# Optimization experiments

Measured on AMD Instinct MI355X. Metric: run time of the kernel, lower is better.

Reference implementation:

```python
import jax, jax.numpy as jnp
import numpy as np

N_NODES = 100000
N_EDGES = 1600000
IN_DIM = 128
HID = 128


def sage_conv(x, src, dst, W_l, W_r, b, num_nodes):
    # PyG SAGEConv (mean aggregation): out = lin_l(mean_{j in N(i)} x_j) + lin_r(x_i)
    msgs = x[src]                                            # [E, F] gather
    agg = jax.ops.segment_sum(msgs, dst, num_segments=num_nodes)  # [N, F]
    cnt = jax.ops.segment_sum(jnp.ones((src.shape[0],), x.dtype), dst,
                              num_segments=num_nodes)        # [N]
    agg = agg / jnp.maximum(cnt, 1.0)[:, None]               # mean; 0 for isolated nodes
    return agg @ W_l + b + x @ W_r


def setup_inputs() -> dict:
    key = jax.random.key(0)
    ks = jax.random.split(key, 12)
    s_in = 1.0 / np.sqrt(IN_DIM)
    s_h = 1.0 / np.sqrt(HID)
    return {
        "x": jax.random.normal(ks[0], (N_NODES, IN_DIM), jnp.float32),
        "edge_index": jax.random.randint(ks[1], (2, N_EDGES), 0, N_NODES, jnp.int64),
        "Wl1": jax.random.normal(ks[2], (IN_DIM, HID), jnp.float32) * s_in,
        "Wr1": jax.random.normal(ks[3], (IN_DIM, HID), jnp.float32) * s_in,
        "b1": jnp.zeros((HID,), jnp.float32),
        "Wl2": jax.random.normal(ks[4], (HID, HID), jnp.float32) * s_h,
        "Wr2": jax.random.normal(ks[5], (HID, HID), jnp.float32) * s_h,
        "b2": jnp.zeros((HID,), jnp.float32),
        "Wp": jax.random.normal(ks[6], (HID, 1), jnp.float32) * s_h,
        "bp": jnp.zeros((1,), jnp.float32),
        "Wd": jax.random.normal(ks[7], (HID, 1), jnp.float32) * s_h,
        "bd": jnp.zeros((1,), jnp.float32),
    }


def reference(x, edge_index, Wl1, Wr1, b1, Wl2, Wr2, b2, Wp, bp, Wd, bd):
    src, dst = edge_index[0], edge_index[1]
    h = jax.nn.relu(sage_conv(x, src, dst, Wl1, Wr1, b1, N_NODES))
    h = jax.nn.relu(sage_conv(h, src, dst, Wl2, Wr2, b2, N_NODES))
    preds = h @ Wp + bp                      # [N, 1]
    diffs = jax.nn.sigmoid(h @ Wd + bd)      # [N, 1]
    return (preds - diffs, preds + diffs)
```

## Files before the change

kernel.cpp:

```cpp
#include <hip/hip_runtime.h>
#include <hip/hip_bf16.h>

#define N_NODES 100000
#define N_EDGES 1600000
#define NBUCK 391
#define BCAP 5120
#define ACHUNK 4096

typedef __bf16 bf16x8 __attribute__((ext_vector_type(8)));
typedef __bf16 bf16x4 __attribute__((ext_vector_type(4)));
typedef float  f32x4  __attribute__((ext_vector_type(4)));
typedef float  f32x2  __attribute__((ext_vector_type(2)));



__global__ __launch_bounds__(512) void zerob_kernel(int* __restrict__ bcnt,
                                                    int* __restrict__ Psent) {
  int t = threadIdx.x;
  if (t < NBUCK) bcnt[t] = 0;
  if (t >= 480) Psent[t - 480] = 0;
}

__global__ __launch_bounds__(256) void partA_kernel(const int* __restrict__ src,
                                                    const int* __restrict__ dst,
                                                    int* __restrict__ bcnt,
                                                    unsigned* __restrict__ packed, int E) {
  __shared__ int hist[NBUCK];
  __shared__ int curs[NBUCK];
  const int t = threadIdx.x;
  for (int i = t; i < NBUCK; i += 256) hist[i] = 0;
  __syncthreads();

  const int base = blockIdx.x * ACHUNK;
  const int lim = min(base + ACHUNK, E);

  int dloc[16], sloc[16];
  int myn = 0;
  for (int i = base + t; i < lim; i += 256) {
    dloc[myn] = dst[i];
    sloc[myn] = src[i];
    ++myn;
  }
  for (int k = 0; k < myn; ++k) atomicAdd(&hist[dloc[k] >> 8], 1);
  __syncthreads();

  for (int i = t; i < NBUCK; i += 256) {
    int h = hist[i];
    curs[i] = (h > 0) ? atomicAdd(&bcnt[i], h) : 0;
  }
  __syncthreads();

  for (int k = 0; k < myn; ++k) {
    int d = dloc[k];
    int b = d >> 8;
    int pos = atomicAdd(&curs[b], 1);
    if (pos < BCAP)
      packed[(size_t)b * BCAP + pos] = ((unsigned)sloc[k] << 8) | (unsigned)(d & 255);
  }
}

__global__ __launch_bounds__(256) void partBh_kernel(const unsigned* __restrict__ packed,
                                                     const int* __restrict__ bcnt,
                                                     int* __restrict__ pcnt,
                                                     int* __restrict__ deg,
                                                     int* __restrict__ pbt, int N) {
  __shared__ int hist[256];
  __shared__ int red[256];
  const int b = blockIdx.x, t = threadIdx.x;
  hist[t] = 0;
  __syncthreads();
  const int ecnt = min(bcnt[b], BCAP);
  const unsigned* pk = packed + (size_t)b * BCAP;
  for (int i = t; i < ecnt; i += 256) atomicAdd(&hist[pk[i] & 255u], 1);
  __syncthreads();
  int c = hist[t];
  int node = b * 256 + t;
  int pc = (node < N) ? ((c + 3) & ~3) : 0;
  if (node < N) { deg[node] = c; pcnt[node] = pc; }
  red[t] = pc;
  __syncthreads();
  for (int d = 128; d > 0; d >>= 1) {
    if (t < d) red[t] += red[t + d];
    __syncthreads();
  }
  if (t == 0) pbt[b] = red[0];
}

__global__ __launch_bounds__(512) void bscan_kernel(const int* __restrict__ pbt,
                                                    int* __restrict__ bbase,
                                                    int* __restrict__ offs, int N) {
  __shared__ int tmp[512];
  int t = threadIdx.x;
  int v = (t < NBUCK) ? pbt[t] : 0;
  int x = v;
  tmp[t] = x;
  __syncthreads();
  for (int d = 1; d < 512; d <<= 1) {
    int y = (t >= d) ? tmp[t - d] : 0;
    __syncthreads();
    x += y;
    tmp[t] = x;
    __syncthreads();
  }
  if (t < NBUCK) bbase[t] = x - v;
  if (t == NBUCK - 1) offs[N] = x;
}

__global__ __launch_bounds__(256) void partBs_kernel(const unsigned* __restrict__ packed,
                                                     const int* __restrict__ bcnt,
                                                     const int* __restrict__ bbase,
                                                     const int* __restrict__ pcnt,
                                                     const int* __restrict__ deg,
                                                     int* __restrict__ offs,
                                                     int* __restrict__ ssrc, int N) {
  __shared__ int scanbuf[256];
  __shared__ int curs[256];
  const int b = blockIdx.x, t = threadIdx.x;
  const int node = b * 256 + t;
  int pc = (node < N) ? pcnt[node] : 0;
  int c  = (node < N) ? deg[node] : 0;
  int x = pc;
  scanbuf[t] = x;
  __syncthreads();
  for (int d = 1; d < 256; d <<= 1) {
    int y = (t >= d) ? scanbuf[t - d] : 0;
    __syncthreads();
    x += y;
    scanbuf[t] = x;
    __syncthreads();
  }
  int excl = x - pc;
  const int obase = bbase[b];
  if (node < N) offs[node] = obase + excl;
  curs[t] = excl;
  __syncthreads();

  const int ecnt = min(bcnt[b], BCAP);
  const unsigned* pk = packed + (size_t)b * BCAP;
  for (int i = t; i < ecnt; i += 256) {
    unsigned p = pk[i];
    int r = atomicAdd(&curs[p & 255u], 1);
    ssrc[obase + r] = (int)(p >> 8);
  }
  for (int j = c; j < pc; ++j) ssrc[obase + excl + j] = N;
}


__global__ __launch_bounds__(256) void wswz_kernel(const float* __restrict__ Wl1,
                                                   const float* __restrict__ Wr1,
                                                   const float* __restrict__ Wl2,
                                                   const float* __restrict__ Wr2,
                                                   __bf16* __restrict__ W1out,
                                                   __bf16* __restrict__ W2out) {
  int gi = blockIdx.x * blockDim.x + threadIdx.x;
  bool L2 = gi >= 32768;
  int i = gi & 32767;
  int j = i & 7;
  int lane = (i >> 3) & 63;
  int c = (i >> 9) & 3;
  int tile = i >> 11;
  int k = c * 32 + ((lane >> 4) * 8) + j;
  int krow = L2 ? (((k & 7) << 4) | (k >> 3)) : k;
  int col = tile * 16 + (lane & 15);
  const float* Wl = L2 ? Wl2 : Wl1;
  const float* Wr = L2 ? Wr2 : Wr1;
  float v = (col < 128) ? Wl[krow * 128 + col] : Wr[krow * 128 + (col - 128)];
  (L2 ? W2out : W1out)[i] = (__bf16)v;
}


template <bool A_IS_F32>
__global__ __launch_bounds__(256, 2) void gemm_kernel(const void* __restrict__ Aptr,
                                                      const __bf16* __restrict__ Wswz,
                                                      const float* __restrict__ bias,
                                                      unsigned char* __restrict__ P,
                                                      __bf16* __restrict__ R, int M,
                                                      int tiles, int stride) {
  const int t = threadIdx.x;
  const int lane = t & 63;
  const int w = t >> 6;
  const int q = lane >> 4;
  const int s = lane & 15;

  bf16x8 bfrag[16];
#pragma unroll
  for (int ct = 0; ct < 4; ++ct)
#pragma unroll
    for (int c = 0; c < 4; ++c)
      bfrag[ct * 4 + c] =
          *(const bf16x8*)&Wswz[(size_t)((((w * 4 + ct) * 4 + c) * 64) + lane) * 8];

  float breg[4];
#pragma unroll
  for (int j = 0; j < 4; ++j)
    breg[j] = (w >= 2) ? bias[((w - 2) * 4 + j) * 16 + s] : 0.f;

  for (int tile = blockIdx.x; tile < tiles; tile += stride) {
    const int m0 = tile * 64;

    bf16x8 afrag[16];
    if (A_IS_F32) {
      const float* A = (const float*)Aptr;
#pragma unroll
      for (int rt = 0; rt < 4; ++rt) {
        int rc = min(m0 + rt * 16 + s, M - 1);
#pragma unroll
        for (int c = 0; c < 4; ++c) {
          const float* p = &A[(size_t)rc * 128 + c * 32 + q * 8];
          float4 v0 = *(const float4*)p;
          float4 v1 = *(const float4*)(p + 4);
          bf16x8 a;
          a[0] = (__bf16)v0.x; a[1] = (__bf16)v0.y; a[2] = (__bf16)v0.z; a[3] = (__bf16)v0.w;
          a[4] = (__bf16)v1.x; a[5] = (__bf16)v1.y; a[6] = (__bf16)v1.z; a[7] = (__bf16)v1.w;
          afrag[rt * 4 + c] = a;
        }
      }
    } else {
      const __bf16* A = (const __bf16*)Aptr;
#pragma unroll
      for (int rt = 0; rt < 4; ++rt) {
        int rc = min(m0 + rt * 16 + s, M - 1);
#pragma unroll
        for (int c = 0; c < 4; ++c)
          afrag[rt * 4 + c] = *(const bf16x8*)&A[(size_t)rc * 128 + c * 32 + q * 8];
      }
    }

    f32x4 acc[16];
    f32x4 zero = {0.f, 0.f, 0.f, 0.f};
#pragma unroll
    for (int i = 0; i < 16; ++i) acc[i] = zero;

#pragma unroll
    for (int c = 0; c < 4; ++c)
#pragma unroll
      for (int rt = 0; rt < 4; ++rt)
#pragma unroll
        for (int ct = 0; ct < 4; ++ct)
          acc[rt * 4 + ct] = __builtin_amdgcn_mfma_f32_16x16x32_bf16(
              afrag[rt * 4 + c], bfrag[ct * 4 + c], acc[rt * 4 + ct], 0, 0, 0);

#pragma unroll
    for (int rt = 0; rt < 4; ++rt) {
#pragma unroll
      for (int r = 0; r < 4; ++r) {
        int row = m0 + rt * 16 + q * 4 + r;
        if (row < M) {
          if (w < 2) {
            unsigned v = 0;
            v = __builtin_amdgcn_cvt_pk_fp8_f32(acc[rt * 4 + 0][r], acc[rt * 4 + 1][r], v, false);
            v = __builtin_amdgcn_cvt_pk_fp8_f32(acc[rt * 4 + 2][r], acc[rt * 4 + 3][r], v, true);
            *(unsigned*)&P[(size_t)row * 128 + s * 8 + w * 4] = v;
          } else {
            bf16x4 o;
#pragma unroll
            for (int ct = 0; ct < 4; ++ct) o[ct] = (__bf16)(acc[rt * 4 + ct][r] + breg[ct]);
            *(bf16x4*)&R[(size_t)row * 128 + s * 8 + (w - 2) * 4] = o;
          }
        }
      }
    }
  }
}


template <bool FINAL>
__global__ __launch_bounds__(256) void agg_kernel(
    const unsigned char* __restrict__ P, const __bf16* R,
    const int* __restrict__ offs, const int* __restrict__ deg,
    const int* __restrict__ ssrc,
    __bf16* H, float* __restrict__ out,
    const float* __restrict__ Wp, const float* __restrict__ Wd,
    const float* __restrict__ bp, const float* __restrict__ bd, int n) {
  int w4 = (int)((blockIdx.x * blockDim.x + threadIdx.x) >> 6);
  int lane = threadIdx.x & 63;
  int g = lane >> 4;
  int s = lane & 15;
  int node = w4 * 4 + g;
  int nc = min(node, n - 1);
  int start = offs[nc];
  int pend = offs[nc + 1];

  f32x2 a01 = {0.f, 0.f}, a23 = {0.f, 0.f}, a45 = {0.f, 0.f}, a67 = {0.f, 0.f};

  const unsigned char* Pb = P + (size_t)s * 8;
  for (int cur = start; cur < pend; cur += 4) {
    uint4 sv = *(const uint4*)&ssrc[cur];
    uint2 v0 = *(const uint2*)(Pb + (size_t)sv.x * 128);
    uint2 v1 = *(const uint2*)(Pb + (size_t)sv.y * 128);
    uint2 v2 = *(const uint2*)(Pb + (size_t)sv.z * 128);
    uint2 v3 = *(const uint2*)(Pb + (size_t)sv.w * 128);
    a01 += __builtin_amdgcn_cvt_pk_f32_fp8(v0.x, false);
    a23 += __builtin_amdgcn_cvt_pk_f32_fp8(v0.x, true);
    a45 += __builtin_amdgcn_cvt_pk_f32_fp8(v0.y, false);
    a67 += __builtin_amdgcn_cvt_pk_f32_fp8(v0.y, true);
    a01 += __builtin_amdgcn_cvt_pk_f32_fp8(v1.x, false);
    a23 += __builtin_amdgcn_cvt_pk_f32_fp8(v1.x, true);
    a45 += __builtin_amdgcn_cvt_pk_f32_fp8(v1.y, false);
    a67 += __builtin_amdgcn_cvt_pk_f32_fp8(v1.y, true);
    a01 += __builtin_amdgcn_cvt_pk_f32_fp8(v2.x, false);
    a23 += __builtin_amdgcn_cvt_pk_f32_fp8(v2.x, true);
    a45 += __builtin_amdgcn_cvt_pk_f32_fp8(v2.y, false);
    a67 += __builtin_amdgcn_cvt_pk_f32_fp8(v2.y, true);
    a01 += __builtin_amdgcn_cvt_pk_f32_fp8(v3.x, false);
    a23 += __builtin_amdgcn_cvt_pk_f32_fp8(v3.x, true);
    a45 += __builtin_amdgcn_cvt_pk_f32_fp8(v3.y, false);
    a67 += __builtin_amdgcn_cvt_pk_f32_fp8(v3.y, true);
  }

  int dg = deg[nc];
  float inv = 1.0f / (float)(dg > 0 ? dg : 1);

  bf16x8 rv = *(const bf16x8*)&R[(size_t)nc * 128 + s * 8];
  float acc[8] = {a01[0], a01[1], a23[0], a23[1], a45[0], a45[1], a67[0], a67[1]};
  float h[8];
#pragma unroll
  for (int j = 0; j < 8; ++j) {
    h[j] = fmaxf(acc[j] * inv + (float)rv[j], 0.f);
  }

  if (!FINAL) {
    if (node < n) {
      bf16x8 o;
#pragma unroll
      for (int j = 0; j < 8; ++j) o[j] = (__bf16)h[j];
      *(bf16x8*)&H[(size_t)node * 128 + s * 8] = o;
    }
  } else {
    float p = 0.f, dd = 0.f;
#pragma unroll
    for (int j = 0; j < 8; ++j) {
      p += h[j] * Wp[j * 16 + s];
      dd += h[j] * Wd[j * 16 + s];
    }
    p += __shfl_xor(p, 1, 64);  p += __shfl_xor(p, 2, 64);
    p += __shfl_xor(p, 4, 64);  p += __shfl_xor(p, 8, 64);
    dd += __shfl_xor(dd, 1, 64); dd += __shfl_xor(dd, 2, 64);
    dd += __shfl_xor(dd, 4, 64); dd += __shfl_xor(dd, 8, 64);
    if (node < n && s == 0) {
      float preds = p + bp[0];
      float sg = 1.0f / (1.0f + __expf(-(dd + bd[0])));
      out[node] = preds - sg;
      out[n + node] = preds + sg;
    }
  }
}


extern "C" void kernel_launch(void* const* d_in, const int* in_sizes, int n_in,
                              void* d_out, int out_size, void* d_ws, size_t ws_size,
                              hipStream_t stream) {
  const float* x    = (const float*)d_in[0];
  const int*   ei   = (const int*)d_in[1];
  const float* Wl1 = (const float*)d_in[2];
  const float* Wr1 = (const float*)d_in[3];
  const float* b1  = (const float*)d_in[4];
  const float* Wl2 = (const float*)d_in[5];
  const float* Wr2 = (const float*)d_in[6];
  const float* b2  = (const float*)d_in[7];
  const float* Wp  = (const float*)d_in[8];
  const float* bp  = (const float*)d_in[9];
  const float* Wd  = (const float*)d_in[10];
  const float* bd  = (const float*)d_in[11];
  float* out = (float*)d_out;

  const int N = N_NODES, E = N_EDGES;
  const int* src = ei;
  const int* dst = ei + E;
  const size_t PADE = (size_t)E + 3 * (size_t)N + 64;

  char* w = (char*)d_ws;
  unsigned char* P = (unsigned char*)w; w += (size_t)(N + 1) * 128;
  __bf16* R1     = (__bf16*)w;   w += (size_t)N * 128 * 2;
  __bf16* R2     = (__bf16*)w;   w += (size_t)N * 128 * 2;
  int* ssrc      = (int*)w;      w += PADE * 4;
  unsigned* pck  = (unsigned*)w; w += (size_t)NBUCK * BCAP * 4;
  int* bcnt      = (int*)w;      w += 512 * 4;
  int* bbase     = (int*)w;      w += 512 * 4;
  int* pbt       = (int*)w;      w += 512 * 4;
  int* pcnt      = (int*)w;      w += (size_t)(N + 32) * 4;
  int* deg       = (int*)w;      w += (size_t)(N + 32) * 4;
  int* offs      = (int*)w;      w += (size_t)(N + 32) * 4;
  __bf16* Ws1    = (__bf16*)w;   w += 65536;
  __bf16* Ws2    = (__bf16*)w;   w += 65536;

  zerob_kernel<<<1, 512, 0, stream>>>(bcnt, (int*)(P + (size_t)N * 128));
  wswz_kernel<<<256, 256, 0, stream>>>(Wl1, Wr1, Wl2, Wr2, Ws1, Ws2);
  partA_kernel<<<(E + ACHUNK - 1) / ACHUNK, 256, 0, stream>>>(src, dst, bcnt, pck, E);
  partBh_kernel<<<NBUCK, 256, 0, stream>>>(pck, bcnt, pcnt, deg, pbt, N);
  bscan_kernel<<<1, 512, 0, stream>>>(pbt, bbase, offs, N);
  partBs_kernel<<<NBUCK, 256, 0, stream>>>(pck, bcnt, bbase, pcnt, deg, offs, ssrc, N);

  const int TILES = (N + 63) / 64;
  const int GG = 512;
  const int AB = (N + 15) / 16;
  gemm_kernel<true><<<GG, 256, 0, stream>>>(x, Ws1, b1, P, R1, N, TILES, GG);
  agg_kernel<false><<<AB, 256, 0, stream>>>(P, R1, offs, deg, ssrc, R1, nullptr,
                                            nullptr, nullptr, nullptr, nullptr, N);
  gemm_kernel<false><<<GG, 256, 0, stream>>>(R1, Ws2, b2, P, R2, N, TILES, GG);
  agg_kernel<true><<<AB, 256, 0, stream>>>(P, R2, offs, deg, ssrc, nullptr, out,
                                           Wp, Wd, bp, bd, N);
}
```

Baseline: 278.9 us.

## Fuse layer-1 aggregation with layer-2 GEMM and stage GEMM1 inputs through LDS

Layer-1 neighbour aggregation and the layer-2 linear transform now run in one persistent kernel. Each block aggregates 16 nodes, stages the hidden rows in LDS and feeds them to MFMA, so the bf16 hidden matrix is never written to or read back from global memory, and one launch disappears. The gather loop issues two groups of 4 neighbour loads per iteration to keep more loads in flight. The first GEMM now loads its fp32 input tile cooperatively into LDS with coalesced float4 reads before building fragments. The trade-off is that the fused kernel runs at launch bound 2 with a fixed 512-block grid-stride, which may leave fewer waves to hide the latency of the random gathers.

```diff
diff --git a/kernel.cpp b/kernel.cpp
--- a/kernel.cpp
+++ b/kernel.cpp
@@ -15,10 +15,11 @@
 
 
 __global__ __launch_bounds__(512) void zerob_kernel(int* __restrict__ bcnt,
-                                                    int* __restrict__ Psent) {
+                                                    int* __restrict__ P1s,
+                                                    int* __restrict__ P2s) {
   int t = threadIdx.x;
   if (t < NBUCK) bcnt[t] = 0;
-  if (t >= 480) Psent[t - 480] = 0;
+  if (t >= 480) { P1s[t - 480] = 0; P2s[t - 480] = 0; }
 }
 
 __global__ __launch_bounds__(256) void partA_kernel(const int* __restrict__ src,
@@ -169,13 +170,13 @@
 }
 
 
-template <bool A_IS_F32>
-__global__ __launch_bounds__(256, 2) void gemm_kernel(const void* __restrict__ Aptr,
-                                                      const __bf16* __restrict__ Wswz,
-                                                      const float* __restrict__ bias,
-                                                      unsigned char* __restrict__ P,
-                                                      __bf16* __restrict__ R, int M,
-                                                      int tiles, int stride) {
+__global__ __launch_bounds__(256, 2) void gemm1_kernel(const float* __restrict__ A,
+                                                       const __bf16* __restrict__ Wswz,
+                                                       const float* __restrict__ bias,
+                                                       unsigned char* __restrict__ P,
+                                                       __bf16* __restrict__ R, int M,
+                                                       int tiles, int stride) {
+  __shared__ __bf16 ldsA[64][136];
   const int t = threadIdx.x;
   const int lane = t & 63;
   const int w = t >> 6;
@@ -198,33 +199,24 @@
   for (int tile = blockIdx.x; tile < tiles; tile += stride) {
     const int m0 = tile * 64;
 
+#pragma unroll
+    for (int it = 0; it < 8; ++it) {
+      int row = it * 8 + (t >> 5);
+      int col = (t & 31) * 4;
+      float4 v = make_float4(0.f, 0.f, 0.f, 0.f);
+      if (m0 + row < M) v = *(const float4*)&A[(size_t)(m0 + row) * 128 + col];
+      bf16x4 bv;
+      bv.x = (__bf16)v.x; bv.y = (__bf16)v.y; bv.z = (__bf16)v.z; bv.w = (__bf16)v.w;
+      *(bf16x4*)&ldsA[row][col] = bv;
+    }
+    __syncthreads();
+
     bf16x8 afrag[16];
-    if (A_IS_F32) {
-      const float* A = (const float*)Aptr;
-#pragma unroll
-      for (int rt = 0; rt < 4; ++rt) {
-        int rc = min(m0 + rt * 16 + s, M - 1);
-#pragma unroll
-        for (int c = 0; c < 4; ++c) {
-          const float* p = &A[(size_t)rc * 128 + c * 32 + q * 8];
-          float4 v0 = *(const float4*)p;
-          float4 v1 = *(const float4*)(p + 4);
-          bf16x8 a;
-          a[0] = (__bf16)v0.x; a[1] = (__bf16)v0.y; a[2] = (__bf16)v0.z; a[3] = (__bf16)v0.w;
-          a[4] = (__bf16)v1.x; a[5] = (__bf16)v1.y; a[6] = (__bf16)v1.z; a[7] = (__bf16)v1.w;
-          afrag[rt * 4 + c] = a;
-        }
-      }
-    } else {
-      const __bf16* A = (const __bf16*)Aptr;
-#pragma unroll
-      for (int rt = 0; rt < 4; ++rt) {
-        int rc = min(m0 + rt * 16 + s, M - 1);
-#pragma unroll
-        for (int c = 0; c < 4; ++c)
-          afrag[rt * 4 + c] = *(const bf16x8*)&A[(size_t)rc * 128 + c * 32 + q * 8];
-      }
-    }
+#pragma unroll
+    for (int rt = 0; rt < 4; ++rt)
+#pragma unroll
+      for (int c = 0; c < 4; ++c)
+        afrag[rt * 4 + c] = *(const bf16x8*)&ldsA[rt * 16 + s][c * 32 + q * 8];
 
     f32x4 acc[16];
     f32x4 zero = {0.f, 0.f, 0.f, 0.f};
@@ -260,16 +252,148 @@
         }
       }
     }
-  }
-}
-
-
-template <bool FINAL>
-__global__ __launch_bounds__(256) void agg_kernel(
-    const unsigned char* __restrict__ P, const __bf16* R,
+    __syncthreads();
+  }
+}
+
+
+__global__ __launch_bounds__(256, 2) void fused_kernel(
+    const unsigned char* __restrict__ P1, __bf16* R,
     const int* __restrict__ offs, const int* __restrict__ deg,
     const int* __restrict__ ssrc,
-    __bf16* H, float* __restrict__ out,
+    const __bf16* __restrict__ Wswz, const float* __restrict__ bias,
+    unsigned char* __restrict__ P2, int n, int ntiles, int stride) {
+  __shared__ __bf16 ldsH[16][136];
+  const int t = threadIdx.x;
+  const int lane = t & 63;
+  const int w = t >> 6;
+  const int q = lane >> 4;
+  const int s = lane & 15;
+
+  bf16x8 bfrag[16];
+#pragma unroll
+  for (int ct = 0; ct < 4; ++ct)
+#pragma unroll
+    for (int c = 0; c < 4; ++c)
+      bfrag[ct * 4 + c] =
+          *(const bf16x8*)&Wswz[(size_t)((((w * 4 + ct) * 4 + c) * 64) + lane) * 8];
+
+  float breg[4];
+#pragma unroll
+  for (int j = 0; j < 4; ++j)
+    breg[j] = (w >= 2) ? bias[((w - 2) * 4 + j) * 16 + s] : 0.f;
+
+  const unsigned char* Pb = P1 + (size_t)s * 8;
+
+  for (int tile = blockIdx.x; tile < ntiles; tile += stride) {
+    int node = tile * 16 + w * 4 + q;
+    int nc = min(node, n - 1);
+    int start = offs[nc];
+    int pend = offs[nc + 1];
+
+    f32x2 a01 = {0.f, 0.f}, a23 = {0.f, 0.f}, a45 = {0.f, 0.f}, a67 = {0.f, 0.f};
+    for (int cur = start; cur < pend; cur += 8) {
+      uint4 sv = *(const uint4*)&ssrc[cur];
+      uint2 v0 = *(const uint2*)(Pb + (size_t)sv.x * 128);
+      uint2 v1 = *(const uint2*)(Pb + (size_t)sv.y * 128);
+      uint2 v2 = *(const uint2*)(Pb + (size_t)sv.z * 128);
+      uint2 v3 = *(const uint2*)(Pb + (size_t)sv.w * 128);
+      if (cur + 4 < pend) {
+        uint4 sw = *(const uint4*)&ssrc[cur + 4];
+        uint2 u0 = *(const uint2*)(Pb + (size_t)sw.x * 128);
+        uint2 u1 = *(const uint2*)(Pb + (size_t)sw.y * 128);
+        uint2 u2 = *(const uint2*)(Pb + (size_t)sw.z * 128);
+        uint2 u3 = *(const uint2*)(Pb + (size_t)sw.w * 128);
+        a01 += __builtin_amdgcn_cvt_pk_f32_fp8(u0.x, false);
+        a23 += __builtin_amdgcn_cvt_pk_f32_fp8(u0.x, true);
+        a45 += __builtin_amdgcn_cvt_pk_f32_fp8(u0.y, false);
+        a67 += __builtin_amdgcn_cvt_pk_f32_fp8(u0.y, true);
+        a01 += __builtin_amdgcn_cvt_pk_f32_fp8(u1.x, false);
+        a23 += __builtin_amdgcn_cvt_pk_f32_fp8(u1.x, true);
+        a45 += __builtin_amdgcn_cvt_pk_f32_fp8(u1.y, false);
+        a67 += __builtin_amdgcn_cvt_pk_f32_fp8(u1.y, true);
+        a01 += __builtin_amdgcn_cvt_pk_f32_fp8(u2.x, false);
+        a23 += __builtin_amdgcn_cvt_pk_f32_fp8(u2.x, true);
+        a45 += __builtin_amdgcn_cvt_pk_f32_fp8(u2.y, false);
+        a67 += __builtin_amdgcn_cvt_pk_f32_fp8(u2.y, true);
+        a01 += __builtin_amdgcn_cvt_pk_f32_fp8(u3.x, false);
+        a23 += __builtin_amdgcn_cvt_pk_f32_fp8(u3.x, true);
+        a45 += __builtin_amdgcn_cvt_pk_f32_fp8(u3.y, false);
+        a67 += __builtin_amdgcn_cvt_pk_f32_fp8(u3.y, true);
+      }
+      a01 += __builtin_amdgcn_cvt_pk_f32_fp8(v0.x, false);
+      a23 += __builtin_amdgcn_cvt_pk_f32_fp8(v0.x, true);
+      a45 += __builtin_amdgcn_cvt_pk_f32_fp8(v0.y, false);
+      a67 += __builtin_amdgcn_cvt_pk_f32_fp8(v0.y, true);
+      a01 += __builtin_amdgcn_cvt_pk_f32_fp8(v1.x, false);
+      a23 += __builtin_amdgcn_cvt_pk_f32_fp8(v1.x, true);
+      a45 += __builtin_amdgcn_cvt_pk_f32_fp8(v1.y, false);
+      a67 += __builtin_amdgcn_cvt_pk_f32_fp8(v1.y, true);
+      a01 += __builtin_amdgcn_cvt_pk_f32_fp8(v2.x, false);
+      a23 += __builtin_amdgcn_cvt_pk_f32_fp8(v2.x, true);
+      a45 += __builtin_amdgcn_cvt_pk_f32_fp8(v2.y, false);
+      a67 += __builtin_amdgcn_cvt_pk_f32_fp8(v2.y, true);
+      a01 += __builtin_amdgcn_cvt_pk_f32_fp8(v3.x, false);
+      a23 += __builtin_amdgcn_cvt_pk_f32_fp8(v3.x, true);
+      a45 += __builtin_amdgcn_cvt_pk_f32_fp8(v3.y, false);
+      a67 += __builtin_amdgcn_cvt_pk_f32_fp8(v3.y, true);
+    }
+
+    int dg = deg[nc];
+    float inv = 1.0f / (float)(dg > 0 ? dg : 1);
+    bf16x8 rv = *(const bf16x8*)&R[(size_t)nc * 128 + s * 8];
+    float acc1[8] = {a01[0], a01[1], a23[0], a23[1], a45[0], a45[1], a67[0], a67[1]};
+    bf16x8 hh;
+#pragma unroll
+    for (int j = 0; j < 8; ++j)
+      hh[j] = (__bf16)fmaxf(acc1[j] * inv + (float)rv[j], 0.f);
+
+    *(bf16x8*)&ldsH[w * 4 + q][s * 8] = hh;
+    __syncthreads();
+
+    bf16x8 afrag[4];
+#pragma unroll
+    for (int c = 0; c < 4; ++c)
+      afrag[c] = *(const bf16x8*)&ldsH[s][c * 32 + q * 8];
+
+    f32x4 acc2[4];
+    f32x4 zero = {0.f, 0.f, 0.f, 0.f};
+#pragma unroll
+    for (int i = 0; i < 4; ++i) acc2[i] = zero;
+
+#pragma unroll
+    for (int c = 0; c < 4; ++c)
+#pragma unroll
+      for (int ct = 0; ct < 4; ++ct)
+        acc2[ct] = __builtin_amdgcn_mfma_f32_16x16x32_bf16(afrag[c], bfrag[ct * 4 + c],
+                                                           acc2[ct], 0, 0, 0);
+
+#pragma unroll
+    for (int r = 0; r < 4; ++r) {
+      int row = tile * 16 + q * 4 + r;
+      if (row < n) {
+        if (w < 2) {
+          unsigned v = 0;
+          v = __builtin_amdgcn_cvt_pk_fp8_f32(acc2[0][r], acc2[1][r], v, false);
+          v = __builtin_amdgcn_cvt_pk_fp8_f32(acc2[2][r], acc2[3][r], v, true);
+          *(unsigned*)&P2[(size_t)row * 128 + s * 8 + w * 4] = v;
+        } else {
+          bf16x4 o;
+#pragma unroll
+          for (int ct = 0; ct < 4; ++ct) o[ct] = (__bf16)(acc2[ct][r] + breg[ct]);
+          *(bf16x4*)&R[(size_t)row * 128 + s * 8 + (w - 2) * 4] = o;
+        }
+      }
+    }
+    __syncthreads();
+  }
+}
+
+
+__global__ __launch_bounds__(256) void agg2_kernel(
+    const unsigned char* __restrict__ P, const __bf16* __restrict__ R,
+    const int* __restrict__ offs, const int* __restrict__ deg,
+    const int* __restrict__ ssrc, float* __restrict__ out,
     const float* __restrict__ Wp, const float* __restrict__ Wd,
     const float* __restrict__ bp, const float* __restrict__ bd, int n) {
   int w4 = (int)((blockIdx.x * blockDim.x + threadIdx.x) >> 6);
@@ -313,36 +437,22 @@
 
   bf16x8 rv = *(const bf16x8*)&R[(size_t)nc * 128 + s * 8];
   float acc[8] = {a01[0], a01[1], a23[0], a23[1], a45[0], a45[1], a67[0], a67[1]};
-  float h[8];
+  float p = 0.f, dd = 0.f;
 #pragma unroll
   for (int j = 0; j < 8; ++j) {
-    h[j] = fmaxf(acc[j] * inv + (float)rv[j], 0.f);
-  }
-
-  if (!FINAL) {
-    if (node < n) {
-      bf16x8 o;
-#pragma unroll
-      for (int j = 0; j < 8; ++j) o[j] = (__bf16)h[j];
-      *(bf16x8*)&H[(size_t)node * 128 + s * 8] = o;
-    }
-  } else {
-    float p = 0.f, dd = 0.f;
-#pragma unroll
-    for (int j = 0; j < 8; ++j) {
-      p += h[j] * Wp[j * 16 + s];
-      dd += h[j] * Wd[j * 16 + s];
-    }
-    p += __shfl_xor(p, 1, 64);  p += __shfl_xor(p, 2, 64);
-    p += __shfl_xor(p, 4, 64);  p += __shfl_xor(p, 8, 64);
-    dd += __shfl_xor(dd, 1, 64); dd += __shfl_xor(dd, 2, 64);
-    dd += __shfl_xor(dd, 4, 64); dd += __shfl_xor(dd, 8, 64);
-    if (node < n && s == 0) {
-      float preds = p + bp[0];
-      float sg = 1.0f / (1.0f + __expf(-(dd + bd[0])));
-      out[node] = preds - sg;
-      out[n + node] = preds + sg;
-    }
+    float h = fmaxf(acc[j] * inv + (float)rv[j], 0.f);
+    p += h * Wp[j * 16 + s];
+    dd += h * Wd[j * 16 + s];
+  }
+  p += __shfl_xor(p, 1, 64);  p += __shfl_xor(p, 2, 64);
+  p += __shfl_xor(p, 4, 64);  p += __shfl_xor(p, 8, 64);
+  dd += __shfl_xor(dd, 1, 64); dd += __shfl_xor(dd, 2, 64);
+  dd += __shfl_xor(dd, 4, 64); dd += __shfl_xor(dd, 8, 64);
+  if (node < n && s == 0) {
+    float preds = p + bp[0];
+    float sg = 1.0f / (1.0f + __expf(-(dd + bd[0])));
+    out[node] = preds - sg;
+    out[n + node] = preds + sg;
   }
 }
 
@@ -370,9 +480,9 @@
   const size_t PADE = (size_t)E + 3 * (size_t)N + 64;
 
   char* w = (char*)d_ws;
-  unsigned char* P = (unsigned char*)w; w += (size_t)(N + 1) * 128;
-  __bf16* R1     = (__bf16*)w;   w += (size_t)N * 128 * 2;
-  __bf16* R2     = (__bf16*)w;   w += (size_t)N * 128 * 2;
+  unsigned char* P1 = (unsigned char*)w; w += (size_t)(N + 1) * 128;
+  unsigned char* P2 = (unsigned char*)w; w += (size_t)(N + 1) * 128;
+  __bf16* Rbuf   = (__bf16*)w;   w += (size_t)N * 128 * 2;
   int* ssrc      = (int*)w;      w += PADE * 4;
   unsigned* pck  = (unsigned*)w; w += (size_t)NBUCK * BCAP * 4;
   int* bcnt      = (int*)w;      w += 512 * 4;
@@ -384,7 +494,8 @@
   __bf16* Ws1    = (__bf16*)w;   w += 65536;
   __bf16* Ws2    = (__bf16*)w;   w += 65536;
 
-  zerob_kernel<<<1, 512, 0, stream>>>(bcnt, (int*)(P + (size_t)N * 128));
+  zerob_kernel<<<1, 512, 0, stream>>>(bcnt, (int*)(P1 + (size_t)N * 128),
+                                      (int*)(P2 + (size_t)N * 128));
   wswz_kernel<<<256, 256, 0, stream>>>(Wl1, Wr1, Wl2, Wr2, Ws1, Ws2);
   partA_kernel<<<(E + ACHUNK - 1) / ACHUNK, 256, 0, stream>>>(src, dst, bcnt, pck, E);
   partBh_kernel<<<NBUCK, 256, 0, stream>>>(pck, bcnt, pcnt, deg, pbt, N);
@@ -392,12 +503,10 @@
   partBs_kernel<<<NBUCK, 256, 0, stream>>>(pck, bcnt, bbase, pcnt, deg, offs, ssrc, N);
 
   const int TILES = (N + 63) / 64;
+  const int NT16  = (N + 15) / 16;
   const int GG = 512;
-  const int AB = (N + 15) / 16;
-  gemm_kernel<true><<<GG, 256, 0, stream>>>(x, Ws1, b1, P, R1, N, TILES, GG);
-  agg_kernel<false><<<AB, 256, 0, stream>>>(P, R1, offs, deg, ssrc, R1, nullptr,
-                                            nullptr, nullptr, nullptr, nullptr, N);
-  gemm_kernel<false><<<GG, 256, 0, stream>>>(R1, Ws2, b2, P, R2, N, TILES, GG);
-  agg_kernel<true><<<AB, 256, 0, stream>>>(P, R2, offs, deg, ssrc, nullptr, out,
-                                           Wp, Wd, bp, bd, N);
-}
+  gemm1_kernel<<<GG, 256, 0, stream>>>(x, Ws1, b1, P1, Rbuf, N, TILES, GG);
+  fused_kernel<<<GG, 256, 0, stream>>>(P1, Rbuf, offs, deg, ssrc, Ws2, b2, P2, N, NT16, GG);
+  agg2_kernel<<<NT16, 256, 0, stream>>>(P2, Rbuf, offs, deg, ssrc, out,
+                                        Wp, Wd, bp, bd, N);
+}
```

New measurement: 278.6 us. About the same (-0.1%).
